# Kernel tuning notes

Measured on AMD Instinct MI355X. Metric: run time of the kernel, lower is better.

Reference implementation:

```python
import jax, jax.numpy as jnp
import numpy as np

B, N, D = 2, 2048, 1024
H = 16
HD = D // H  # 64
NEG = -1e30


def setup_inputs() -> dict:
    key = jax.random.key(0)
    ks = jax.random.split(key, 6)
    s = 0.02
    return {
        "x": jax.random.normal(ks[0], (B, N, D), dtype=jnp.float32),
        "Wq": jax.random.normal(ks[1], (D, D), dtype=jnp.float32) * s,
        "Wk": jax.random.normal(ks[2], (D, D), dtype=jnp.float32) * s,
        "Wv": jax.random.normal(ks[3], (D, D), dtype=jnp.float32) * s,
        "Wo": jax.random.normal(ks[4], (D, D), dtype=jnp.float32) * s,
        "Wf": jax.random.normal(ks[5], (D, H), dtype=jnp.float32) * s,
    }


def reference(x, Wq, Wk, Wv, Wo, Wf):
    b, n, d = x.shape
    h, hd = H, HD
    scale = hd ** -0.5
    # projections (Linear without bias; weights stored as [in, out])
    q = (x @ Wq).reshape(b, n, h, hd).transpose(0, 2, 1, 3)  # b h n hd
    k = (x @ Wk).reshape(b, n, h, hd).transpose(0, 2, 1, 3)
    v = (x @ Wv).reshape(b, n, h, hd).transpose(0, 2, 1, 3)
    # per-head log forget gate, cumulative sum over positions
    log_f = jax.nn.log_sigmoid(x @ Wf).transpose(0, 2, 1)  # b h n
    c = jnp.cumsum(log_f, axis=-1)  # b h n
    # scores with additive decay bias: bias[i,j] = c[i] - c[j] (j <= i)
    scores = jnp.einsum('bhid,bhjd->bhij', q, k) * scale
    scores = scores + c[..., :, None] - c[..., None, :]
    causal = jnp.tril(jnp.ones((n, n), dtype=bool))
    scores = jnp.where(causal, scores, NEG)
    attn = jax.nn.softmax(scores, axis=-1)
    out = jnp.einsum('bhij,bhjd->bhid', attn, v)  # b h n hd
    out = out.transpose(0, 2, 1, 3).reshape(b, n, d)
    return out @ Wo
```

## Files before the change

kernel.cpp:

```cpp
#include <hip/hip_runtime.h>
#include <hip/hip_bf16.h>
#include <stdint.h>

#define NN 2048
#define DD 1024
#define HH 16
#define HDD 64
#define QBLK 64
#define KVBLK 64

typedef unsigned short u16;
typedef __attribute__((ext_vector_type(8))) __bf16 bf16x8_t;
typedef __attribute__((ext_vector_type(4))) float f32x4_t;

static __device__ __forceinline__ u16 f2bf(float f) {
  union { float f; uint32_t u; } v; v.f = f;
  uint32_t r = v.u + 0x7FFFu + ((v.u >> 16) & 1u);
  return (u16)(r >> 16);
}

static __device__ __forceinline__ uint32_t packbf2(float a, float b) {
  __hip_bfloat162 h2 = __float22bfloat162_rn(make_float2(a, b));
  union { __hip_bfloat162 hh; uint32_t u; } cvt; cvt.hh = h2;
  return cvt.u;
}

static __device__ __forceinline__ void async_copy16(const void* g, void* l) {
  __builtin_amdgcn_global_load_lds((const __attribute__((address_space(1))) void*)g,
                                   (__attribute__((address_space(3))) void*)l, 16, 0, 0);
}

__global__ void transpose_w_kernel(const float* __restrict__ W0, const float* __restrict__ W1,
                                   const float* __restrict__ W2, const float* __restrict__ W3,
                                   u16* __restrict__ Wt) {
  __shared__ float tile[64][65];
  const float* W = blockIdx.y == 0 ? W0 : blockIdx.y == 1 ? W1 : blockIdx.y == 2 ? W2 : W3;
  u16* out = Wt + (size_t)blockIdx.y * DD * DD;
  int bx = blockIdx.x & 15;
  int by = blockIdx.x >> 4;
  int t = threadIdx.x;
  int c = t & 63, r4 = t >> 6;
#pragma unroll
  for (int i = 0; i < 16; i++) {
    int row = i * 4 + r4;
    tile[row][c] = W[(by * 64 + row) * DD + bx * 64 + c];
  }
  __syncthreads();
#pragma unroll
  for (int i = 0; i < 16; i++) {
    int row = i * 4 + r4;
    out[(bx * 64 + row) * DD + by * 64 + c] = f2bf(tile[c][row]);
  }
}

__global__ void logf_kernel(const float* __restrict__ x, const float* __restrict__ Wf,
                            float* __restrict__ lf, u16* __restrict__ xb) {
  __shared__ float xs[DD];
  __shared__ float part[16][17];
  int row = blockIdx.x;
  int t = threadIdx.x;
  float4 v = *(const float4*)&x[(size_t)row * DD + t * 4];
  *(float4*)&xs[t * 4] = v;
  ushort4 o;
  o.x = f2bf(v.x); o.y = f2bf(v.y); o.z = f2bf(v.z); o.w = f2bf(v.w);
  *(ushort4*)&xb[(size_t)row * DD + t * 4] = o;
  __syncthreads();
  int h = t & 15, chunk = t >> 4;
  float s = 0.f;
#pragma unroll 8
  for (int e = 0; e < 64; e++)
    s += xs[chunk * 64 + e] * Wf[(chunk * 64 + e) * HH + h];
  part[chunk][h] = s;
  __syncthreads();
  if (t < 16) {
    float z = 0.f;
#pragma unroll
    for (int i = 0; i < 16; i++) z += part[i][t];
    float ls = fminf(z, 0.f) - log1pf(__expf(-fabsf(z)));
    int b = row >> 11, n = row & (NN - 1);
    lf[(b * HH + t) * NN + n] = ls;
  }
}

__global__ void cumsum_kernel(const float* __restrict__ lf, float* __restrict__ c) {
  int bh = blockIdx.x;
  int lane = threadIdx.x;
  const float* in = lf + bh * NN;
  float* out = c + bh * NN;
  float carry = 0.f;
  for (int t0 = 0; t0 < NN; t0 += 256) {
    float4 v = *(const float4*)&in[t0 + lane * 4];
    float s1 = v.x + v.y, s2 = s1 + v.z, s3 = s2 + v.w;
    float incl = s3;
#pragma unroll
    for (int off = 1; off < 64; off <<= 1) {
      float u = __shfl_up(incl, off, 64);
      if (lane >= off) incl += u;
    }
    float excl = incl - s3 + carry;
    float4 o;
    o.x = excl + v.x; o.y = excl + s1; o.z = excl + s2; o.w = excl + s3;
    *(float4*)&out[t0 + lane * 4] = o;
    carry = __shfl(incl, 63, 64) + carry;
  }
}

__global__ __launch_bounds__(512, 4) void gemm_kernel(const u16* __restrict__ A,
                                                      const u16* __restrict__ Wt,
                                                      u16* __restrict__ oQ, u16* __restrict__ oK,
                                                      u16* __restrict__ oV, float* __restrict__ oF,
                                                      int mode) {
  __shared__ u16 Als[128 * 64];
  __shared__ u16 Bls[128 * 64];
  int m0 = blockIdx.y * 128, n0 = blockIdx.x * 128;
  int tid = threadIdx.x;
  int lane = tid & 63, w = tid >> 6;
  int wm = w >> 2, wn = w & 3;
  int lr = lane & 15, lg = lane >> 4;

  const u16* gA[2]; const u16* gB[2]; u16* lA[2]; u16* lB[2];
#pragma unroll
  for (int j = 0; j < 2; j++) {
    int s = tid + j * 512;
    int row = s >> 3, ch = s & 7;
    int scol = (ch ^ (row & 7)) * 8;
    gA[j] = &A [(size_t)(m0 + row) * DD + scol];
    gB[j] = &Wt[(size_t)(n0 + row) * DD + scol];
    lA[j] = &Als[s * 8];
    lB[j] = &Bls[s * 8];
  }

  f32x4_t acc[4][2];
#pragma unroll
  for (int i = 0; i < 4; i++)
#pragma unroll
    for (int j = 0; j < 2; j++) acc[i][j] = (f32x4_t){0.f, 0.f, 0.f, 0.f};

  for (int kt = 0; kt < DD; kt += 64) {
    __syncthreads();
#pragma unroll
    for (int j = 0; j < 2; j++) {
      async_copy16(gA[j] + kt, lA[j]);
      async_copy16(gB[j] + kt, lB[j]);
    }
    __syncthreads();
#pragma unroll
    for (int kk = 0; kk < 2; kk++) {
      bf16x8_t af[4], bfv[2];
#pragma unroll
      for (int mi = 0; mi < 4; mi++) {
        int row = wm * 64 + mi * 16 + lr;
        int boff = (row * 128 + kk * 64 + lg * 16) ^ ((row & 7) << 4);
        af[mi] = *(const bf16x8_t*)((const char*)Als + boff);
      }
#pragma unroll
      for (int ni = 0; ni < 2; ni++) {
        int row = wn * 32 + ni * 16 + lr;
        int boff = (row * 128 + kk * 64 + lg * 16) ^ ((row & 7) << 4);
        bfv[ni] = *(const bf16x8_t*)((const char*)Bls + boff);
      }
#pragma unroll
      for (int mi = 0; mi < 4; mi++)
#pragma unroll
        for (int ni = 0; ni < 2; ni++)
          acc[mi][ni] = __builtin_amdgcn_mfma_f32_16x16x32_bf16(af[mi], bfv[ni], acc[mi][ni], 0, 0, 0);
    }
  }

  if (mode == 1) {
#pragma unroll
    for (int mi = 0; mi < 4; mi++)
#pragma unroll
      for (int ni = 0; ni < 2; ni++) {
        int gcol = n0 + wn * 32 + ni * 16 + lr;
#pragma unroll
        for (int r = 0; r < 4; r++) {
          int grow = m0 + wm * 64 + mi * 16 + lg * 4 + r;
          oF[(size_t)grow * DD + gcol] = acc[mi][ni][r];
        }
      }
  } else {
    int which = n0 >> 10;
    u16* outp = which == 0 ? oQ : which == 1 ? oK : oV;
    int nl0 = n0 & 1023;
#pragma unroll
    for (int mi = 0; mi < 4; mi++)
#pragma unroll
      for (int ni = 0; ni < 2; ni++) {
        int gcol = nl0 + wn * 32 + ni * 16 + lr;
        int h = gcol >> 6, hd = gcol & 63;
#pragma unroll
        for (int r = 0; r < 4; r++) {
          int grow = m0 + wm * 64 + mi * 16 + lg * 4 + r;
          int b = grow >> 11, n = grow & (NN - 1);
          outp[((size_t)(b * HH + h) * NN + n) * HDD + hd] = f2bf(acc[mi][ni][r]);
        }
      }
  }
}

__global__ void transpose_v_kernel(const u16* __restrict__ Vtmp, u16* __restrict__ Vt) {
  __shared__ u16 tile[64][80];
  int bh = blockIdx.y;
  int n0 = blockIdx.x * 64;
  int t = threadIdx.x;
  const u16* src = Vtmp + (size_t)bh * NN * HDD;
  u16* dst = Vt + (size_t)bh * HDD * NN;
#pragma unroll
  for (int it = 0; it < 2; it++) {
    int cc = t + it * 256;
    int row = cc >> 3, p = cc & 7;
    *(uint4*)&tile[row][p * 8] = *(const uint4*)&src[(size_t)(n0 + row) * HDD + p * 8];
  }
  __syncthreads();
#pragma unroll
  for (int it = 0; it < 2; it++) {
    int cc = t + it * 256;
    int row = cc >> 3, p = cc & 7;
    union { u16 v[8]; uint4 q; } tmp;
#pragma unroll
    for (int e = 0; e < 8; e++) tmp.v[e] = tile[p * 8 + e][row];
    *(uint4*)&dst[(size_t)row * NN + n0 + p * 8] = tmp.q;
  }
}

__global__ __launch_bounds__(256) void attn_kernel(const u16* __restrict__ Q,
                                                   const u16* __restrict__ K,
                                                   const u16* __restrict__ Vt,
                                                   const float* __restrict__ cw,
                                                   u16* __restrict__ O) {
  __shared__ u16 Kls[2][KVBLK * 64];
  __shared__ u16 Vls[2][64 * KVBLK];
  int flat = blockIdx.y * gridDim.x + blockIdx.x;
  int swz = (flat & 7) * 64 + (flat >> 3);
  int pidx = swz & 15, bh = swz >> 4;
  int tid = threadIdx.x;
  int lane = tid & 63, w = tid >> 6;
  int lr = lane & 15, lg = lane >> 4;
  const u16* Qh = Q + (size_t)bh * NN * HDD;
  const u16* Kh = K + (size_t)bh * NN * HDD;
  const u16* Vh = Vt + (size_t)bh * HDD * NN;
  const float* ch = cw + bh * NN;
  int b = bh >> 4, h = bh & 15;

  int s0 = tid, s1 = tid + 256;
  int r0 = s0 >> 3, p0 = s0 & 7;
  int r1 = s1 >> 3, p1 = s1 & 7;
  const u16* gk0 = &Kh[(size_t)r0 * HDD + ((p0 ^ (r0 & 7)) * 8)];
  const u16* gk1 = &Kh[(size_t)r1 * HDD + ((p1 ^ (r1 & 7)) * 8)];
  const u16* gv0 = &Vh[(size_t)r0 * NN + ((p0 ^ (r0 & 7)) * 8)];
  const u16* gv1 = &Vh[(size_t)r1 * NN + ((p1 ^ (r1 & 7)) * 8)];

  for (int which = 0; which < 2; which++) {
    int tile = which == 0 ? (31 - pidx) : pidx;
    int qb = tile * QBLK + w * 16;
    int iq = qb + lr;

    bf16x8_t qf[2];
#pragma unroll
    for (int s = 0; s < 2; s++)
      qf[s] = *(const bf16x8_t*)&Qh[(size_t)iq * HDD + s * 32 + lg * 8];
    float cq = ch[iq];

    float lsum = 0.f;
    f32x4_t oacc[4];
#pragma unroll
    for (int fn = 0; fn < 4; fn++) oacc[fn] = (f32x4_t){0.f, 0.f, 0.f, 0.f};

    async_copy16(gk0, &Kls[0][s0 * 8]);
    async_copy16(gk1, &Kls[0][s1 * 8]);
    async_copy16(gv0, &Vls[0][s0 * 8]);
    async_copy16(gv1, &Vls[0][s1 * 8]);
    __syncthreads();

    int cur = 0;
    for (int kvt = 0; kvt <= tile; kvt++) {
      if (kvt < tile) {
        int nb = cur ^ 1;
        size_t kvn = (size_t)(kvt + 1) * KVBLK;
        async_copy16(gk0 + kvn * HDD, &Kls[nb][s0 * 8]);
        async_copy16(gk1 + kvn * HDD, &Kls[nb][s1 * 8]);
        async_copy16(gv0 + kvn, &Vls[nb][s0 * 8]);
        async_copy16(gv1 + kvn, &Vls[nb][s1 * 8]);
      }
      int kv0 = kvt * KVBLK;
      const u16* Kb = Kls[cur];
      const u16* Vb = Vls[cur];
      float4 ckv[4];
#pragma unroll
      for (int f = 0; f < 4; f++)
        ckv[f] = *(const float4*)&ch[kv0 + f * 16 + lg * 4];

      f32x4_t sacc[4];
#pragma unroll
      for (int f = 0; f < 4; f++) sacc[f] = (f32x4_t){0.f, 0.f, 0.f, 0.f};
      __builtin_amdgcn_s_setprio(1);
#pragma unroll
      for (int f = 0; f < 4; f++) {
        int row = f * 16 + lr;
#pragma unroll
        for (int s = 0; s < 2; s++) {
          int boff = (row * 128 + s * 64 + lg * 16) ^ ((row & 7) << 4);
          bf16x8_t kf = *(const bf16x8_t*)((const char*)Kb + boff);
          sacc[f] = __builtin_amdgcn_mfma_f32_16x16x32_bf16(kf, qf[s], sacc[f], 0, 0, 0);
        }
      }
      __builtin_amdgcn_s_setprio(0);

      bool diag = (kvt == tile);
      float pv[4][4];
#pragma unroll
      for (int f = 0; f < 4; f++) {
        const float* ckp = &ckv[f].x;
#pragma unroll
        for (int r = 0; r < 4; r++) {
          float val = fmaf(sacc[f][r], 0.125f, cq - ckp[r]);
          float e = __expf(val);
          if (diag && (kv0 + f * 16 + lg * 4 + r) > iq) e = 0.f;
          pv[f][r] = e; lsum += e;
        }
      }

      uint32_t wq[4][2];
#pragma unroll
      for (int f = 0; f < 4; f++) {
        wq[f][0] = packbf2(pv[f][0], pv[f][1]);
        wq[f][1] = packbf2(pv[f][2], pv[f][3]);
      }
      bf16x8_t pa[2];
#pragma unroll
      for (int s = 0; s < 2; s++) {
        uint32_t x0 = wq[2 * s][0], x1 = wq[2 * s][1];
        uint32_t y0 = wq[2 * s + 1][0], y1 = wq[2 * s + 1][1];
        asm volatile("v_permlane32_swap_b32 %0, %1" : "+v"(x0), "+v"(y0));
        asm volatile("v_permlane32_swap_b32 %0, %1" : "+v"(x1), "+v"(y1));
        asm volatile("v_permlane16_swap_b32 %0, %1" : "+v"(x0), "+v"(y0));
        asm volatile("v_permlane16_swap_b32 %0, %1" : "+v"(x1), "+v"(y1));
        union { uint32_t u[4]; bf16x8_t v; } pk;
        pk.u[0] = x0; pk.u[1] = x1; pk.u[2] = y0; pk.u[3] = y1;
        pa[s] = pk.v;
      }

      __builtin_amdgcn_s_setprio(1);
#pragma unroll
      for (int fn = 0; fn < 4; fn++) {
        int row = fn * 16 + lr;
#pragma unroll
        for (int s = 0; s < 2; s++) {
          int boff = (row * 128 + s * 64 + lg * 16) ^ ((row & 7) << 4);
          bf16x8_t vf = *(const bf16x8_t*)((const char*)Vb + boff);
          oacc[fn] = __builtin_amdgcn_mfma_f32_16x16x32_bf16(vf, pa[s], oacc[fn], 0, 0, 0);
        }
      }
      __builtin_amdgcn_s_setprio(0);
      __syncthreads();
      cur ^= 1;
    }

    lsum += __shfl_xor(lsum, 16, 64);
    lsum += __shfl_xor(lsum, 32, 64);
    float rinv = 1.0f / lsum;

    u16* orow = O + ((size_t)(b * NN + iq)) * DD + h * HDD;
#pragma unroll
    for (int fn = 0; fn < 4; fn++) {
      ushort4 o4;
      o4.x = f2bf(oacc[fn][0] * rinv);
      o4.y = f2bf(oacc[fn][1] * rinv);
      o4.z = f2bf(oacc[fn][2] * rinv);
      o4.w = f2bf(oacc[fn][3] * rinv);
      *(ushort4*)&orow[fn * 16 + lg * 4] = o4;
    }
  }
}

extern "C" void kernel_launch(void* const* d_in, const int* in_sizes, int n_in,
                              void* d_out, int out_size, void* d_ws, size_t ws_size,
                              hipStream_t stream) {
  const float* x  = (const float*)d_in[0];
  const float* Wq = (const float*)d_in[1];
  const float* Wk = (const float*)d_in[2];
  const float* Wv = (const float*)d_in[3];
  const float* Wo = (const float*)d_in[4];
  const float* Wf = (const float*)d_in[5];
  float* out = (float*)d_out;
  char* ws = (char*)d_ws;
  const size_t MB = 1024 * 1024;
  u16* x_bf  = (u16*)(ws + 0);
  u16* WqkvT = (u16*)(ws + 8 * MB);
  u16* WoT   = (u16*)(ws + 14 * MB);
  u16* Qw    = (u16*)(ws + 16 * MB);
  u16* Kw    = (u16*)(ws + 24 * MB);
  u16* Vw    = (u16*)(ws + 32 * MB);
  u16* Ow    = (u16*)(ws + 40 * MB);
  float* lf  = (float*)(ws + 48 * MB);
  float* cwp = (float*)(ws + 48 * MB + 262144);
  u16* Vtmp  = (u16*)(ws + 49 * MB);

  transpose_w_kernel<<<dim3(256, 4), 256, 0, stream>>>(Wq, Wk, Wv, Wo, WqkvT);
  logf_kernel<<<4096, 256, 0, stream>>>(x, Wf, lf, x_bf);
  cumsum_kernel<<<32, 64, 0, stream>>>(lf, cwp);
  gemm_kernel<<<dim3(24, 32), 512, 0, stream>>>(x_bf, WqkvT, Qw, Kw, Vtmp, nullptr, 0);
  transpose_v_kernel<<<dim3(32, 32), 256, 0, stream>>>(Vtmp, Vw);
  attn_kernel<<<dim3(16, 32), 256, 0, stream>>>(Qw, Kw, Vw, cwp, Ow);
  gemm_kernel<<<dim3(8, 32), 512, 0, stream>>>(Ow, WqkvT + (size_t)3 * DD * DD, nullptr, nullptr, nullptr, out, 1);
}
```

Before: 129.8 us.

## Load K/V fragments directly from global into registers, drop LDS staging

Replaces the shared-memory double buffer for K and V tiles with per-lane register double buffering that loads MFMA operand fragments straight from global memory, prefetching the next tile during compute. This removes the LDS writes and reads and the per-iteration block barrier. In exchange each of the four waves now fetches the full K/V tile independently, so global/L2 traffic per block rises about fourfold, and register pressure grows with two 16-fragment buffers.

```diff
diff --git a/kernel.cpp b/kernel.cpp
--- a/kernel.cpp
+++ b/kernel.cpp
@@ -224,13 +224,13 @@
   }
 }
 
+struct KVfrag { bf16x8_t k[4][2]; bf16x8_t v[4][2]; };
+
 __global__ __launch_bounds__(256) void attn_kernel(const u16* __restrict__ Q,
                                                    const u16* __restrict__ K,
                                                    const u16* __restrict__ Vt,
                                                    const float* __restrict__ cw,
                                                    u16* __restrict__ O) {
-  __shared__ u16 Kls[2][KVBLK * 64];
-  __shared__ u16 Vls[2][64 * KVBLK];
   int flat = blockIdx.y * gridDim.x + blockIdx.x;
   int swz = (flat & 7) * 64 + (flat >> 3);
   int pidx = swz & 15, bh = swz >> 4;
@@ -243,13 +243,8 @@
   const float* ch = cw + bh * NN;
   int b = bh >> 4, h = bh & 15;
 
-  int s0 = tid, s1 = tid + 256;
-  int r0 = s0 >> 3, p0 = s0 & 7;
-  int r1 = s1 >> 3, p1 = s1 & 7;
-  const u16* gk0 = &Kh[(size_t)r0 * HDD + ((p0 ^ (r0 & 7)) * 8)];
-  const u16* gk1 = &Kh[(size_t)r1 * HDD + ((p1 ^ (r1 & 7)) * 8)];
-  const u16* gv0 = &Vh[(size_t)r0 * NN + ((p0 ^ (r0 & 7)) * 8)];
-  const u16* gv1 = &Vh[(size_t)r1 * NN + ((p1 ^ (r1 & 7)) * 8)];
+  const u16* kbase = Kh + lr * HDD + lg * 8;
+  const u16* vbase = Vh + (size_t)lr * NN + lg * 8;
 
   for (int which = 0; which < 2; which++) {
     int tile = which == 0 ? (31 - pidx) : pidx;
@@ -267,25 +262,27 @@
 #pragma unroll
     for (int fn = 0; fn < 4; fn++) oacc[fn] = (f32x4_t){0.f, 0.f, 0.f, 0.f};
 
-    async_copy16(gk0, &Kls[0][s0 * 8]);
-    async_copy16(gk1, &Kls[0][s1 * 8]);
-    async_copy16(gv0, &Vls[0][s0 * 8]);
-    async_copy16(gv1, &Vls[0][s1 * 8]);
-    __syncthreads();
-
-    int cur = 0;
-    for (int kvt = 0; kvt <= tile; kvt++) {
+    KVfrag bufA, bufB;
+#pragma unroll
+    for (int f = 0; f < 4; f++)
+#pragma unroll
+      for (int s = 0; s < 2; s++) {
+        bufA.k[f][s] = *(const bf16x8_t*)(kbase + (f * 16) * HDD + s * 32);
+        bufA.v[f][s] = *(const bf16x8_t*)(vbase + (size_t)f * 16 * NN + s * 32);
+      }
+
+    auto body = [&](int kvt, KVfrag& cur, KVfrag& nxt) {
+      int kv0 = kvt * KVBLK;
       if (kvt < tile) {
-        int nb = cur ^ 1;
-        size_t kvn = (size_t)(kvt + 1) * KVBLK;
-        async_copy16(gk0 + kvn * HDD, &Kls[nb][s0 * 8]);
-        async_copy16(gk1 + kvn * HDD, &Kls[nb][s1 * 8]);
-        async_copy16(gv0 + kvn, &Vls[nb][s0 * 8]);
-        async_copy16(gv1 + kvn, &Vls[nb][s1 * 8]);
-      }
-      int kv0 = kvt * KVBLK;
-      const u16* Kb = Kls[cur];
-      const u16* Vb = Vls[cur];
+        int kn0 = kv0 + KVBLK;
+#pragma unroll
+        for (int f = 0; f < 4; f++)
+#pragma unroll
+          for (int s = 0; s < 2; s++) {
+            nxt.k[f][s] = *(const bf16x8_t*)(kbase + (size_t)(kn0 + f * 16) * HDD + s * 32);
+            nxt.v[f][s] = *(const bf16x8_t*)(vbase + (size_t)f * 16 * NN + kn0 + s * 32);
+          }
+      }
       float4 ckv[4];
 #pragma unroll
       for (int f = 0; f < 4; f++)
@@ -296,15 +293,10 @@
       for (int f = 0; f < 4; f++) sacc[f] = (f32x4_t){0.f, 0.f, 0.f, 0.f};
       __builtin_amdgcn_s_setprio(1);
 #pragma unroll
-      for (int f = 0; f < 4; f++) {
-        int row = f * 16 + lr;
-#pragma unroll
-        for (int s = 0; s < 2; s++) {
-          int boff = (row * 128 + s * 64 + lg * 16) ^ ((row & 7) << 4);
-          bf16x8_t kf = *(const bf16x8_t*)((const char*)Kb + boff);
-          sacc[f] = __builtin_amdgcn_mfma_f32_16x16x32_bf16(kf, qf[s], sacc[f], 0, 0, 0);
-        }
-      }
+      for (int f = 0; f < 4; f++)
+#pragma unroll
+        for (int s = 0; s < 2; s++)
+          sacc[f] = __builtin_amdgcn_mfma_f32_16x16x32_bf16(cur.k[f][s], qf[s], sacc[f], 0, 0, 0);
       __builtin_amdgcn_s_setprio(0);
 
       bool diag = (kvt == tile);
@@ -343,18 +335,16 @@
 
       __builtin_amdgcn_s_setprio(1);
 #pragma unroll
-      for (int fn = 0; fn < 4; fn++) {
-        int row = fn * 16 + lr;
-#pragma unroll
-        for (int s = 0; s < 2; s++) {
-          int boff = (row * 128 + s * 64 + lg * 16) ^ ((row & 7) << 4);
-          bf16x8_t vf = *(const bf16x8_t*)((const char*)Vb + boff);
-          oacc[fn] = __builtin_amdgcn_mfma_f32_16x16x32_bf16(vf, pa[s], oacc[fn], 0, 0, 0);
-        }
-      }
+      for (int fn = 0; fn < 4; fn++)
+#pragma unroll
+        for (int s = 0; s < 2; s++)
+          oacc[fn] = __builtin_amdgcn_mfma_f32_16x16x32_bf16(cur.v[fn][s], pa[s], oacc[fn], 0, 0, 0);
       __builtin_amdgcn_s_setprio(0);
-      __syncthreads();
-      cur ^= 1;
+    };
+
+    for (int kvt = 0; kvt <= tile;) {
+      body(kvt, bufA, bufB); kvt++;
+      if (kvt <= tile) { body(kvt, bufB, bufA); kvt++; }
     }
 
     lsum += __shfl_xor(lsum, 16, 64);
```

Result: slower. 214.4 us (+65.2%).

## Process paired causal query tiles concurrently in one 512-thread block sharing KV loads

Applied to the files above, without the earlier changes.

Instead of each 256-thread block walking the long and short query tiles one after the other, the attention kernel now runs 512 threads: waves 0-3 take tile 31-p and waves 4-7 take tile p. Both halves share the same double-buffered K/V LDS stream, which is loaded once for the longer tile's range, with each thread now copying one chunk instead of two. The goal is to remove redundant KV loads for the short tile and expose more waves per block for latency hiding. In exchange, waves on the short tile sit idle at the barriers for the rest of the loop, and launch bounds now ask for 4 blocks of 512 threads per CU, which constrains registers.

```diff
diff --git a/kernel.cpp b/kernel.cpp
--- a/kernel.cpp
+++ b/kernel.cpp
@@ -224,16 +224,16 @@
   }
 }
 
-__global__ __launch_bounds__(256) void attn_kernel(const u16* __restrict__ Q,
-                                                   const u16* __restrict__ K,
-                                                   const u16* __restrict__ Vt,
-                                                   const float* __restrict__ cw,
-                                                   u16* __restrict__ O) {
+__global__ __launch_bounds__(512, 4) void attn_kernel(const u16* __restrict__ Q,
+                                                      const u16* __restrict__ K,
+                                                      const u16* __restrict__ Vt,
+                                                      const float* __restrict__ cw,
+                                                      u16* __restrict__ O) {
   __shared__ u16 Kls[2][KVBLK * 64];
   __shared__ u16 Vls[2][64 * KVBLK];
   int flat = blockIdx.y * gridDim.x + blockIdx.x;
   int swz = (flat & 7) * 64 + (flat >> 3);
-  int pidx = swz & 15, bh = swz >> 4;
+  int p = swz & 15, bh = swz >> 4;
   int tid = threadIdx.x;
   int lane = tid & 63, w = tid >> 6;
   int lr = lane & 15, lg = lane >> 4;
@@ -243,46 +243,38 @@
   const float* ch = cw + bh * NN;
   int b = bh >> 4, h = bh & 15;
 
-  int s0 = tid, s1 = tid + 256;
-  int r0 = s0 >> 3, p0 = s0 & 7;
-  int r1 = s1 >> 3, p1 = s1 & 7;
+  int tile = (w < 4) ? (31 - p) : p;
+  int qb = tile * QBLK + (w & 3) * 16;
+  int iq = qb + lr;
+
+  int r0 = tid >> 3, p0 = tid & 7;
   const u16* gk0 = &Kh[(size_t)r0 * HDD + ((p0 ^ (r0 & 7)) * 8)];
-  const u16* gk1 = &Kh[(size_t)r1 * HDD + ((p1 ^ (r1 & 7)) * 8)];
   const u16* gv0 = &Vh[(size_t)r0 * NN + ((p0 ^ (r0 & 7)) * 8)];
-  const u16* gv1 = &Vh[(size_t)r1 * NN + ((p1 ^ (r1 & 7)) * 8)];
-
-  for (int which = 0; which < 2; which++) {
-    int tile = which == 0 ? (31 - pidx) : pidx;
-    int qb = tile * QBLK + w * 16;
-    int iq = qb + lr;
-
-    bf16x8_t qf[2];
-#pragma unroll
-    for (int s = 0; s < 2; s++)
-      qf[s] = *(const bf16x8_t*)&Qh[(size_t)iq * HDD + s * 32 + lg * 8];
-    float cq = ch[iq];
-
-    float lsum = 0.f;
-    f32x4_t oacc[4];
-#pragma unroll
-    for (int fn = 0; fn < 4; fn++) oacc[fn] = (f32x4_t){0.f, 0.f, 0.f, 0.f};
-
-    async_copy16(gk0, &Kls[0][s0 * 8]);
-    async_copy16(gk1, &Kls[0][s1 * 8]);
-    async_copy16(gv0, &Vls[0][s0 * 8]);
-    async_copy16(gv1, &Vls[0][s1 * 8]);
-    __syncthreads();
-
-    int cur = 0;
-    for (int kvt = 0; kvt <= tile; kvt++) {
-      if (kvt < tile) {
-        int nb = cur ^ 1;
-        size_t kvn = (size_t)(kvt + 1) * KVBLK;
-        async_copy16(gk0 + kvn * HDD, &Kls[nb][s0 * 8]);
-        async_copy16(gk1 + kvn * HDD, &Kls[nb][s1 * 8]);
-        async_copy16(gv0 + kvn, &Vls[nb][s0 * 8]);
-        async_copy16(gv1 + kvn, &Vls[nb][s1 * 8]);
-      }
+
+  bf16x8_t qf[2];
+#pragma unroll
+  for (int s = 0; s < 2; s++)
+    qf[s] = *(const bf16x8_t*)&Qh[(size_t)iq * HDD + s * 32 + lg * 8];
+  float cq = ch[iq];
+
+  float lsum = 0.f;
+  f32x4_t oacc[4];
+#pragma unroll
+  for (int fn = 0; fn < 4; fn++) oacc[fn] = (f32x4_t){0.f, 0.f, 0.f, 0.f};
+
+  async_copy16(gk0, &Kls[0][tid * 8]);
+  async_copy16(gv0, &Vls[0][tid * 8]);
+  __syncthreads();
+
+  int ntiles = 32 - p;
+  int cur = 0;
+  for (int kvt = 0; kvt < ntiles; kvt++) {
+    if (kvt + 1 < ntiles) {
+      size_t kvn = (size_t)(kvt + 1) * KVBLK;
+      async_copy16(gk0 + kvn * HDD, &Kls[cur ^ 1][tid * 8]);
+      async_copy16(gv0 + kvn, &Vls[cur ^ 1][tid * 8]);
+    }
+    if (kvt <= tile) {
       int kv0 = kvt * KVBLK;
       const u16* Kb = Kls[cur];
       const u16* Vb = Vls[cur];
@@ -353,24 +345,24 @@
         }
       }
       __builtin_amdgcn_s_setprio(0);
-      __syncthreads();
-      cur ^= 1;
-    }
-
-    lsum += __shfl_xor(lsum, 16, 64);
-    lsum += __shfl_xor(lsum, 32, 64);
-    float rinv = 1.0f / lsum;
-
-    u16* orow = O + ((size_t)(b * NN + iq)) * DD + h * HDD;
-#pragma unroll
-    for (int fn = 0; fn < 4; fn++) {
-      ushort4 o4;
-      o4.x = f2bf(oacc[fn][0] * rinv);
-      o4.y = f2bf(oacc[fn][1] * rinv);
-      o4.z = f2bf(oacc[fn][2] * rinv);
-      o4.w = f2bf(oacc[fn][3] * rinv);
-      *(ushort4*)&orow[fn * 16 + lg * 4] = o4;
-    }
+    }
+    __syncthreads();
+    cur ^= 1;
+  }
+
+  lsum += __shfl_xor(lsum, 16, 64);
+  lsum += __shfl_xor(lsum, 32, 64);
+  float rinv = 1.0f / lsum;
+
+  u16* orow = O + ((size_t)(b * NN + iq)) * DD + h * HDD;
+#pragma unroll
+  for (int fn = 0; fn < 4; fn++) {
+    ushort4 o4;
+    o4.x = f2bf(oacc[fn][0] * rinv);
+    o4.y = f2bf(oacc[fn][1] * rinv);
+    o4.z = f2bf(oacc[fn][2] * rinv);
+    o4.w = f2bf(oacc[fn][3] * rinv);
+    *(ushort4*)&orow[fn * 16 + lg * 4] = o4;
   }
 }
 
@@ -402,6 +394,6 @@
   cumsum_kernel<<<32, 64, 0, stream>>>(lf, cwp);
   gemm_kernel<<<dim3(24, 32), 512, 0, stream>>>(x_bf, WqkvT, Qw, Kw, Vtmp, nullptr, 0);
   transpose_v_kernel<<<dim3(32, 32), 256, 0, stream>>>(Vtmp, Vw);
-  attn_kernel<<<dim3(16, 32), 256, 0, stream>>>(Qw, Kw, Vw, cwp, Ow);
+  attn_kernel<<<dim3(16, 32), 512, 0, stream>>>(Qw, Kw, Vw, cwp, Ow);
   gemm_kernel<<<dim3(8, 32), 512, 0, stream>>>(Ow, WqkvT + (size_t)3 * DD * DD, nullptr, nullptr, nullptr, out, 1);
 }
```

Result: slower. 136.8 us (+5.4%).

## Enlarge attention query tile to 128 rows with two row groups per wave

Applied to the files above, without the earlier changes.

The attention kernel now gives each block one 128-row query tile and each wave two 16-row query groups. Every K/V tile staged in LDS therefore feeds twice as many MFMAs, where before each block looped over a paired short and long 64-row tile. The cumulative log-gate is pre-scaled by log2(e) so exp2f can replace __expf, and the grid is remapped to a 1D swizzle with launch_bounds(256,2). The cost is higher register pressure from doubled accumulators, and a fully masked waste tile for waves whose rows sit early in the block.

```diff
diff --git a/kernel.cpp b/kernel.cpp
--- a/kernel.cpp
+++ b/kernel.cpp
@@ -6,12 +6,13 @@
 #define DD 1024
 #define HH 16
 #define HDD 64
-#define QBLK 64
 #define KVBLK 64
 
 typedef unsigned short u16;
 typedef __attribute__((ext_vector_type(8))) __bf16 bf16x8_t;
 typedef __attribute__((ext_vector_type(4))) float f32x4_t;
+
+#define LOG2E 1.44269504f
 
 static __device__ __forceinline__ u16 f2bf(float f) {
   union { float f; uint32_t u; } v; v.f = f;
@@ -99,7 +100,8 @@
     }
     float excl = incl - s3 + carry;
     float4 o;
-    o.x = excl + v.x; o.y = excl + s1; o.z = excl + s2; o.w = excl + s3;
+    o.x = (excl + v.x) * LOG2E; o.y = (excl + s1) * LOG2E;
+    o.z = (excl + s2) * LOG2E; o.w = (excl + s3) * LOG2E;
     *(float4*)&out[t0 + lane * 4] = o;
     carry = __shfl(incl, 63, 64) + carry;
   }
@@ -224,16 +226,21 @@
   }
 }
 
-__global__ __launch_bounds__(256) void attn_kernel(const u16* __restrict__ Q,
-                                                   const u16* __restrict__ K,
-                                                   const u16* __restrict__ Vt,
-                                                   const float* __restrict__ cw,
-                                                   u16* __restrict__ O) {
+__global__ __launch_bounds__(256, 2) void attn_kernel(const u16* __restrict__ Q,
+                                                      const u16* __restrict__ K,
+                                                      const u16* __restrict__ Vt,
+                                                      const float* __restrict__ cw,
+                                                      u16* __restrict__ O) {
   __shared__ u16 Kls[2][KVBLK * 64];
   __shared__ u16 Vls[2][64 * KVBLK];
-  int flat = blockIdx.y * gridDim.x + blockIdx.x;
-  int swz = (flat & 7) * 64 + (flat >> 3);
-  int pidx = swz & 15, bh = swz >> 4;
+  int flat = blockIdx.x;
+  int x = flat & 7;
+  int i = flat >> 3;
+  int half = i >> 5;
+  int j = i & 31;
+  int bh = x * 4 + (j & 3);
+  int th = j >> 2;
+  int tile = half ? th : (15 - th);
   int tid = threadIdx.x;
   int lane = tid & 63, w = tid >> 6;
   int lr = lane & 15, lg = lane >> 4;
@@ -243,6 +250,11 @@
   const float* ch = cw + bh * NN;
   int b = bh >> 4, h = bh & 15;
 
+  int qb = tile * 128 + w * 32;
+  int iq0 = qb + lr, iq1 = qb + 16 + lr;
+  int tdiag = qb >> 6;
+  int ntiles = 2 * tile + 2;
+
   int s0 = tid, s1 = tid + 256;
   int r0 = s0 >> 3, p0 = s0 & 7;
   int r1 = s1 >> 3, p1 = s1 & 7;
@@ -251,38 +263,40 @@
   const u16* gv0 = &Vh[(size_t)r0 * NN + ((p0 ^ (r0 & 7)) * 8)];
   const u16* gv1 = &Vh[(size_t)r1 * NN + ((p1 ^ (r1 & 7)) * 8)];
 
-  for (int which = 0; which < 2; which++) {
-    int tile = which == 0 ? (31 - pidx) : pidx;
-    int qb = tile * QBLK + w * 16;
-    int iq = qb + lr;
-
-    bf16x8_t qf[2];
-#pragma unroll
-    for (int s = 0; s < 2; s++)
-      qf[s] = *(const bf16x8_t*)&Qh[(size_t)iq * HDD + s * 32 + lg * 8];
-    float cq = ch[iq];
-
-    float lsum = 0.f;
-    f32x4_t oacc[4];
-#pragma unroll
-    for (int fn = 0; fn < 4; fn++) oacc[fn] = (f32x4_t){0.f, 0.f, 0.f, 0.f};
-
-    async_copy16(gk0, &Kls[0][s0 * 8]);
-    async_copy16(gk1, &Kls[0][s1 * 8]);
-    async_copy16(gv0, &Vls[0][s0 * 8]);
-    async_copy16(gv1, &Vls[0][s1 * 8]);
-    __syncthreads();
-
-    int cur = 0;
-    for (int kvt = 0; kvt <= tile; kvt++) {
-      if (kvt < tile) {
-        int nb = cur ^ 1;
-        size_t kvn = (size_t)(kvt + 1) * KVBLK;
-        async_copy16(gk0 + kvn * HDD, &Kls[nb][s0 * 8]);
-        async_copy16(gk1 + kvn * HDD, &Kls[nb][s1 * 8]);
-        async_copy16(gv0 + kvn, &Vls[nb][s0 * 8]);
-        async_copy16(gv1 + kvn, &Vls[nb][s1 * 8]);
-      }
+  bf16x8_t qf0[2], qf1[2];
+#pragma unroll
+  for (int s = 0; s < 2; s++) {
+    qf0[s] = *(const bf16x8_t*)&Qh[(size_t)iq0 * HDD + s * 32 + lg * 8];
+    qf1[s] = *(const bf16x8_t*)&Qh[(size_t)iq1 * HDD + s * 32 + lg * 8];
+  }
+  float cq0 = ch[iq0], cq1 = ch[iq1];
+
+  float lsum0 = 0.f, lsum1 = 0.f;
+  f32x4_t oacc0[4], oacc1[4];
+#pragma unroll
+  for (int fn = 0; fn < 4; fn++) {
+    oacc0[fn] = (f32x4_t){0.f, 0.f, 0.f, 0.f};
+    oacc1[fn] = (f32x4_t){0.f, 0.f, 0.f, 0.f};
+  }
+
+  const float SCL = 0.125f * LOG2E;
+
+  async_copy16(gk0, &Kls[0][s0 * 8]);
+  async_copy16(gk1, &Kls[0][s1 * 8]);
+  async_copy16(gv0, &Vls[0][s0 * 8]);
+  async_copy16(gv1, &Vls[0][s1 * 8]);
+  __syncthreads();
+
+  int cur = 0;
+  for (int kvt = 0; kvt < ntiles; kvt++) {
+    if (kvt + 1 < ntiles) {
+      size_t kvn = (size_t)(kvt + 1) * KVBLK;
+      async_copy16(gk0 + kvn * HDD, &Kls[cur ^ 1][s0 * 8]);
+      async_copy16(gk1 + kvn * HDD, &Kls[cur ^ 1][s1 * 8]);
+      async_copy16(gv0 + kvn, &Vls[cur ^ 1][s0 * 8]);
+      async_copy16(gv1 + kvn, &Vls[cur ^ 1][s1 * 8]);
+    }
+    if (kvt <= tdiag) {
       int kv0 = kvt * KVBLK;
       const u16* Kb = Kls[cur];
       const u16* Vb = Vls[cur];
@@ -291,9 +305,12 @@
       for (int f = 0; f < 4; f++)
         ckv[f] = *(const float4*)&ch[kv0 + f * 16 + lg * 4];
 
-      f32x4_t sacc[4];
-#pragma unroll
-      for (int f = 0; f < 4; f++) sacc[f] = (f32x4_t){0.f, 0.f, 0.f, 0.f};
+      f32x4_t sa0[4], sa1[4];
+#pragma unroll
+      for (int f = 0; f < 4; f++) {
+        sa0[f] = (f32x4_t){0.f, 0.f, 0.f, 0.f};
+        sa1[f] = (f32x4_t){0.f, 0.f, 0.f, 0.f};
+      }
       __builtin_amdgcn_s_setprio(1);
 #pragma unroll
       for (int f = 0; f < 4; f++) {
@@ -302,43 +319,58 @@
         for (int s = 0; s < 2; s++) {
           int boff = (row * 128 + s * 64 + lg * 16) ^ ((row & 7) << 4);
           bf16x8_t kf = *(const bf16x8_t*)((const char*)Kb + boff);
-          sacc[f] = __builtin_amdgcn_mfma_f32_16x16x32_bf16(kf, qf[s], sacc[f], 0, 0, 0);
+          sa0[f] = __builtin_amdgcn_mfma_f32_16x16x32_bf16(kf, qf0[s], sa0[f], 0, 0, 0);
+          sa1[f] = __builtin_amdgcn_mfma_f32_16x16x32_bf16(kf, qf1[s], sa1[f], 0, 0, 0);
         }
       }
       __builtin_amdgcn_s_setprio(0);
 
-      bool diag = (kvt == tile);
-      float pv[4][4];
+      bool diag = (kvt == tdiag);
+      float pv0[4][4], pv1[4][4];
 #pragma unroll
       for (int f = 0; f < 4; f++) {
         const float* ckp = &ckv[f].x;
 #pragma unroll
         for (int r = 0; r < 4; r++) {
-          float val = fmaf(sacc[f][r], 0.125f, cq - ckp[r]);
-          float e = __expf(val);
-          if (diag && (kv0 + f * 16 + lg * 4 + r) > iq) e = 0.f;
-          pv[f][r] = e; lsum += e;
-        }
-      }
-
-      uint32_t wq[4][2];
-#pragma unroll
-      for (int f = 0; f < 4; f++) {
-        wq[f][0] = packbf2(pv[f][0], pv[f][1]);
-        wq[f][1] = packbf2(pv[f][2], pv[f][3]);
-      }
-      bf16x8_t pa[2];
+          int jj = kv0 + f * 16 + lg * 4 + r;
+          float e0 = exp2f(fmaf(sa0[f][r], SCL, cq0 - ckp[r]));
+          float e1 = exp2f(fmaf(sa1[f][r], SCL, cq1 - ckp[r]));
+          if (diag && jj > iq0) e0 = 0.f;
+          if (diag && jj > iq1) e1 = 0.f;
+          pv0[f][r] = e0; lsum0 += e0;
+          pv1[f][r] = e1; lsum1 += e1;
+        }
+      }
+
+      bf16x8_t pa0[2], pa1[2];
 #pragma unroll
       for (int s = 0; s < 2; s++) {
-        uint32_t x0 = wq[2 * s][0], x1 = wq[2 * s][1];
-        uint32_t y0 = wq[2 * s + 1][0], y1 = wq[2 * s + 1][1];
-        asm volatile("v_permlane32_swap_b32 %0, %1" : "+v"(x0), "+v"(y0));
-        asm volatile("v_permlane32_swap_b32 %0, %1" : "+v"(x1), "+v"(y1));
-        asm volatile("v_permlane16_swap_b32 %0, %1" : "+v"(x0), "+v"(y0));
-        asm volatile("v_permlane16_swap_b32 %0, %1" : "+v"(x1), "+v"(y1));
-        union { uint32_t u[4]; bf16x8_t v; } pk;
-        pk.u[0] = x0; pk.u[1] = x1; pk.u[2] = y0; pk.u[3] = y1;
-        pa[s] = pk.v;
+        {
+          uint32_t x0 = packbf2(pv0[2 * s][0], pv0[2 * s][1]);
+          uint32_t x1 = packbf2(pv0[2 * s][2], pv0[2 * s][3]);
+          uint32_t y0 = packbf2(pv0[2 * s + 1][0], pv0[2 * s + 1][1]);
+          uint32_t y1 = packbf2(pv0[2 * s + 1][2], pv0[2 * s + 1][3]);
+          asm volatile("v_permlane32_swap_b32 %0, %1" : "+v"(x0), "+v"(y0));
+          asm volatile("v_permlane32_swap_b32 %0, %1" : "+v"(x1), "+v"(y1));
+          asm volatile("v_permlane16_swap_b32 %0, %1" : "+v"(x0), "+v"(y0));
+          asm volatile("v_permlane16_swap_b32 %0, %1" : "+v"(x1), "+v"(y1));
+          union { uint32_t u[4]; bf16x8_t v; } pk;
+          pk.u[0] = x0; pk.u[1] = x1; pk.u[2] = y0; pk.u[3] = y1;
+          pa0[s] = pk.v;
+        }
+        {
+          uint32_t x0 = packbf2(pv1[2 * s][0], pv1[2 * s][1]);
+          uint32_t x1 = packbf2(pv1[2 * s][2], pv1[2 * s][3]);
+          uint32_t y0 = packbf2(pv1[2 * s + 1][0], pv1[2 * s + 1][1]);
+          uint32_t y1 = packbf2(pv1[2 * s + 1][2], pv1[2 * s + 1][3]);
+          asm volatile("v_permlane32_swap_b32 %0, %1" : "+v"(x0), "+v"(y0));
+          asm volatile("v_permlane32_swap_b32 %0, %1" : "+v"(x1), "+v"(y1));
+          asm volatile("v_permlane16_swap_b32 %0, %1" : "+v"(x0), "+v"(y0));
+          asm volatile("v_permlane16_swap_b32 %0, %1" : "+v"(x1), "+v"(y1));
+          union { uint32_t u[4]; bf16x8_t v; } pk;
+          pk.u[0] = x0; pk.u[1] = x1; pk.u[2] = y0; pk.u[3] = y1;
+          pa1[s] = pk.v;
+        }
       }
 
       __builtin_amdgcn_s_setprio(1);
@@ -349,28 +381,38 @@
         for (int s = 0; s < 2; s++) {
           int boff = (row * 128 + s * 64 + lg * 16) ^ ((row & 7) << 4);
           bf16x8_t vf = *(const bf16x8_t*)((const char*)Vb + boff);
-          oacc[fn] = __builtin_amdgcn_mfma_f32_16x16x32_bf16(vf, pa[s], oacc[fn], 0, 0, 0);
+          oacc0[fn] = __builtin_amdgcn_mfma_f32_16x16x32_bf16(vf, pa0[s], oacc0[fn], 0, 0, 0);
+          oacc1[fn] = __builtin_amdgcn_mfma_f32_16x16x32_bf16(vf, pa1[s], oacc1[fn], 0, 0, 0);
         }
       }
       __builtin_amdgcn_s_setprio(0);
-      __syncthreads();
-      cur ^= 1;
     }
-
-    lsum += __shfl_xor(lsum, 16, 64);
-    lsum += __shfl_xor(lsum, 32, 64);
-    float rinv = 1.0f / lsum;
-
-    u16* orow = O + ((size_t)(b * NN + iq)) * DD + h * HDD;
-#pragma unroll
-    for (int fn = 0; fn < 4; fn++) {
-      ushort4 o4;
-      o4.x = f2bf(oacc[fn][0] * rinv);
-      o4.y = f2bf(oacc[fn][1] * rinv);
-      o4.z = f2bf(oacc[fn][2] * rinv);
-      o4.w = f2bf(oacc[fn][3] * rinv);
-      *(ushort4*)&orow[fn * 16 + lg * 4] = o4;
-    }
+    __syncthreads();
+    cur ^= 1;
+  }
+
+  lsum0 += __shfl_xor(lsum0, 16, 64);
+  lsum0 += __shfl_xor(lsum0, 32, 64);
+  lsum1 += __shfl_xor(lsum1, 16, 64);
+  lsum1 += __shfl_xor(lsum1, 32, 64);
+  float rinv0 = 1.0f / lsum0, rinv1 = 1.0f / lsum1;
+
+  u16* orow0 = O + ((size_t)(b * NN + iq0)) * DD + h * HDD;
+  u16* orow1 = O + ((size_t)(b * NN + iq1)) * DD + h * HDD;
+#pragma unroll
+  for (int fn = 0; fn < 4; fn++) {
+    ushort4 o4;
+    o4.x = f2bf(oacc0[fn][0] * rinv0);
+    o4.y = f2bf(oacc0[fn][1] * rinv0);
+    o4.z = f2bf(oacc0[fn][2] * rinv0);
+    o4.w = f2bf(oacc0[fn][3] * rinv0);
+    *(ushort4*)&orow0[fn * 16 + lg * 4] = o4;
+    ushort4 o5;
+    o5.x = f2bf(oacc1[fn][0] * rinv1);
+    o5.y = f2bf(oacc1[fn][1] * rinv1);
+    o5.z = f2bf(oacc1[fn][2] * rinv1);
+    o5.w = f2bf(oacc1[fn][3] * rinv1);
+    *(ushort4*)&orow1[fn * 16 + lg * 4] = o5;
   }
 }
 
@@ -402,6 +444,6 @@
   cumsum_kernel<<<32, 64, 0, stream>>>(lf, cwp);
   gemm_kernel<<<dim3(24, 32), 512, 0, stream>>>(x_bf, WqkvT, Qw, Kw, Vtmp, nullptr, 0);
   transpose_v_kernel<<<dim3(32, 32), 256, 0, stream>>>(Vtmp, Vw);
-  attn_kernel<<<dim3(16, 32), 256, 0, stream>>>(Qw, Kw, Vw, cwp, Ow);
+  attn_kernel<<<512, 256, 0, stream>>>(Qw, Kw, Vw, cwp, Ow);
   gemm_kernel<<<dim3(8, 32), 512, 0, stream>>>(Ow, WqkvT + (size_t)3 * DD * DD, nullptr, nullptr, nullptr, out, 1);
 }
```

Measured after the change: 154.2 us. 1.19x slower.
